# Kernel optimization log

Measured on AMD Instinct MI355X. Metric: run time of the kernel, lower is better.

Reference implementation:

```python
import jax, jax.numpy as jnp
import numpy as np

B, CIN, T, H, W = 4, 3, 32, 64, 64
COUT = 64


def setup_inputs() -> dict:
    key = jax.random.key(0)
    ks = jax.random.split(key, 6)
    X = jax.random.normal(ks[0], (B, CIN, T, H, W), jnp.float32)
    # Conv3d weight (O, I, D, kH, kW) for kernel (2,3,3)
    Wconv = jax.random.normal(ks[1], (4 * COUT, CIN, 2, 3, 3), jnp.float32) * 0.1
    bconv = jax.random.normal(ks[2], (4 * COUT,), jnp.float32) * 0.1
    # QRNNCell peephole params, shape (out_channels, *frame_size)
    W_ci = jax.random.normal(ks[3], (COUT, H, W), jnp.float32) * 0.1
    W_cf = jax.random.normal(ks[4], (COUT, H, W), jnp.float32) * 0.1
    W_co = jax.random.normal(ks[5], (COUT, H, W), jnp.float32) * 0.1
    return {"X": X, "Wconv": Wconv, "bconv": bconv,
            "W_ci": W_ci, "W_cf": W_cf, "W_co": W_co}


def reference(X, Wconv, bconv, W_ci, W_cf, W_co):
    # ConstantPad3d((1,1,1,1,1,0)): W +-1, H +-1, time front +1
    Xp = jnp.pad(X, ((0, 0), (0, 0), (1, 0), (1, 1), (1, 1)))
    # Conv3d, kernel (2,3,3), VALID -> output (B, 4*COUT, T, H, W)
    E = jax.lax.conv_general_dilated(
        Xp, Wconv, window_strides=(1, 1, 1), padding='VALID',
        dimension_numbers=('NCDHW', 'OIDHW', 'NCDHW'))
    E = E + bconv[None, :, None, None, None]
    i_c, f_c, g_c, o_c = jnp.split(E, 4, axis=1)  # each (B, COUT, T, H, W)
    # time-major stacked gates: (T, 4, B, COUT, H, W)
    gates = jnp.stack([jnp.moveaxis(x, 2, 0) for x in (i_c, f_c, g_c, o_c)], axis=1)

    def step(carry, g4):
        Hs, Cs = carry
        i, f, g, o = g4[0], g4[1], g4[2], g4[3]
        ig = jax.nn.sigmoid(i + W_ci * Cs)
        fg = jax.nn.sigmoid(f + W_cf * Cs)
        Cn = fg * Cs + ig * jnp.tanh(g)
        og = jax.nn.sigmoid(o + W_co * Cn)
        Hn = og * jnp.tanh(Cn)
        return (Hn, Cn), Hn

    z = jnp.zeros((X.shape[0], W_ci.shape[0], X.shape[3], X.shape[4]), X.dtype)
    _, outs = jax.lax.scan(step, (z, z), gates)  # outs: (T, B, COUT, H, W)
    return jnp.moveaxis(outs, 0, 2)  # (B, COUT, T, H, W)
```

## Files before the change

### kernel.cpp

```cpp
#include <hip/hip_runtime.h>

#define TT     32
#define HW     4096
#define LROW   68
#define LPLANE (6 * LROW)
#define SXSZ   (3 * LPLANE)
#define NSTG   (3 * 6 * 66)

__device__ __forceinline__ float fsigmoid(float x) {
    return __builtin_amdgcn_rcpf(1.0f + __builtin_amdgcn_exp2f(x * -1.4426950408889634f));
}
__device__ __forceinline__ float ftanh(float x) {
    return 2.0f * __builtin_amdgcn_rcpf(1.0f + __builtin_amdgcn_exp2f(x * -2.8853900817779268f)) - 1.0f;
}
__device__ __forceinline__ float sgprf(float v) {
    return __uint_as_float(__builtin_amdgcn_readfirstlane(__float_as_uint(v)));
}

__global__ __launch_bounds__(256, 4) void convqrnn(
    const float* __restrict__ X,
    const float* __restrict__ Wc,
    const float* __restrict__ bc,
    const float* __restrict__ Wci,
    const float* __restrict__ Wcf,
    const float* __restrict__ Wco,
    float* __restrict__ out)
{
    __shared__ float sx[2 * SXSZ];
    __shared__ float gb[2 * 1024];

    const int tid = threadIdx.x;
    const int h0  = blockIdx.x * 4;
    const int co  = blockIdx.y;
    const int b   = blockIdx.z;

    const int g  = tid >> 6;
    const int l  = tid & 63;
    const int r  = l >> 4;
    const int c0 = (l & 15) * 4;

    const int prow = tid >> 6;
    const int pcol = tid & 63;
    const int opix = (h0 + prow) * 64 + pcol;

    const float wci = Wci[co * HW + opix];
    const float wcf = Wcf[co * HW + opix];
    const float wco = Wco[co * HW + opix];

    float wgt[54];
    {
        const float* __restrict__ wrow = Wc + (size_t)(g * 64 + co) * 54;
        #pragma unroll
        for (int j = 0; j < 54; ++j) wgt[j] = sgprf(wrow[j]);
    }
    const float bg = sgprf(bc[g * 64 + co]);

    const float* __restrict__ Xb = X + (size_t)b * (3 * TT * HW);
    int soff[5];
    int goff[5];
    int svmask = 0;
    #pragma unroll
    for (int k = 0; k < 5; ++k) {
        int idx  = tid + k * 256;
        bool inr = (idx < NSTG);
        int idc  = inr ? idx : 0;
        int ci   = idc / 396;
        int rem  = idc - ci * 396;
        int y    = rem / 66;
        int x    = rem - y * 66;
        int gh   = h0 + y - 1;
        int gw   = x - 1;
        bool v   = inr && (gh >= 0) && (gh < 64) && (gw >= 0) && (gw < 64);
        int ghc  = gh < 0 ? 0 : (gh > 63 ? 63 : gh);
        int gwc  = gw < 0 ? 0 : (gw > 63 ? 63 : gw);
        soff[k]  = inr ? (ci * LPLANE + y * LROW + x) : (LROW - 1);
        goff[k]  = ci * (TT * HW) + ghc * 64 + gwc;
        svmask  |= (v ? 1 : 0) << k;
    }

    #pragma unroll
    for (int k = 0; k < 5; ++k) {
        float v = ((svmask >> k) & 1) ? Xb[goff[k]] : 0.0f;
        sx[soff[k]] = v;
        goff[k] += HW;
    }

    float* __restrict__ outb = out + (size_t)(b * 64 + co) * (TT * HW);
    int ooff = opix;

    float s0c0 = 0.f, s0c1 = 0.f, s0c2 = 0.f, s0c3 = 0.f;
    float C = 0.f;

    __syncthreads();

    for (int t = 0; t < TT; ++t) {
        const float* __restrict__ sxb = &sx[(t & 1) * SXSZ];
        float*       __restrict__ gbb = &gb[(t & 1) * 1024];

        float win[3][3][6];
        #pragma unroll
        for (int ci = 0; ci < 3; ++ci)
            #pragma unroll
            for (int kh = 0; kh < 3; ++kh) {
                const float* rowp = &sxb[ci * LPLANE + (r + kh) * LROW + c0];
                float4 lo = *(const float4*)rowp;
                float2 hi = *(const float2*)(rowp + 4);
                win[ci][kh][0] = lo.x; win[ci][kh][1] = lo.y;
                win[ci][kh][2] = lo.z; win[ci][kh][3] = lo.w;
                win[ci][kh][4] = hi.x; win[ci][kh][5] = hi.y;
            }

        float stv[5];
        if (t < TT - 1) {
            #pragma unroll
            for (int k = 0; k < 5; ++k) {
                stv[k] = ((svmask >> k) & 1) ? Xb[goff[k]] : 0.0f;
                goff[k] += HW;
            }
        }

        float s10 = bg, s11 = bg, s12 = bg, s13 = bg;
        float n0 = 0.f, n1 = 0.f, n2 = 0.f, n3 = 0.f;
        #pragma unroll
        for (int ci = 0; ci < 3; ++ci)
            #pragma unroll
            for (int kh = 0; kh < 3; ++kh)
                #pragma unroll
                for (int kw = 0; kw < 3; ++kw) {
                    const float wp = wgt[ci * 18 +     kh * 3 + kw];
                    const float wc = wgt[ci * 18 + 9 + kh * 3 + kw];
                    s10 += wc * win[ci][kh][kw + 0];
                    s11 += wc * win[ci][kh][kw + 1];
                    s12 += wc * win[ci][kh][kw + 2];
                    s13 += wc * win[ci][kh][kw + 3];
                    n0  += wp * win[ci][kh][kw + 0];
                    n1  += wp * win[ci][kh][kw + 1];
                    n2  += wp * win[ci][kh][kw + 2];
                    n3  += wp * win[ci][kh][kw + 3];
                }

        float4 gv = make_float4(s10 + s0c0, s11 + s0c1, s12 + s0c2, s13 + s0c3);
        s0c0 = n0; s0c1 = n1; s0c2 = n2; s0c3 = n3;
        *(float4*)&gbb[g * 256 + r * 64 + c0] = gv;

        if (t < TT - 1) {
            float* __restrict__ sxn = &sx[((t + 1) & 1) * SXSZ];
            #pragma unroll
            for (int k = 0; k < 5; ++k) sxn[soff[k]] = stv[k];
        }

        __syncthreads();

        const float iv = gbb[tid];
        const float fv = gbb[256 + tid];
        const float gg = gbb[512 + tid];
        const float ov = gbb[768 + tid];
        const float ig = fsigmoid(iv + wci * C);
        const float fg = fsigmoid(fv + wcf * C);
        const float Cn = fg * C + ig * ftanh(gg);
        const float og = fsigmoid(ov + wco * Cn);
        outb[ooff] = og * ftanh(Cn);
        ooff += HW;
        C = Cn;
    }
}

extern "C" void kernel_launch(void* const* d_in, const int* in_sizes, int n_in,
                              void* d_out, int out_size, void* d_ws, size_t ws_size,
                              hipStream_t stream) {
    const float* X   = (const float*)d_in[0];
    const float* Wc  = (const float*)d_in[1];
    const float* bc  = (const float*)d_in[2];
    const float* Wci = (const float*)d_in[3];
    const float* Wcf = (const float*)d_in[4];
    const float* Wco = (const float*)d_in[5];
    float* out = (float*)d_out;

    dim3 grid(16, 64, 4);
    convqrnn<<<grid, 256, 0, stream>>>(X, Wc, bc, Wci, Wcf, Wco, out);
}
```

Before: 462.7 us.

## Process two output channels per block to reuse staged input window

```diff
diff --git a/kernel.cpp b/kernel.cpp
--- a/kernel.cpp
+++ b/kernel.cpp
@@ -27,11 +27,11 @@
     float* __restrict__ out)
 {
     __shared__ float sx[2 * SXSZ];
-    __shared__ float gb[2 * 1024];
+    __shared__ float gb[2 * 2048];
 
     const int tid = threadIdx.x;
     const int h0  = blockIdx.x * 4;
-    const int co  = blockIdx.y;
+    const int co0 = blockIdx.y * 2;
     const int b   = blockIdx.z;
 
     const int g  = tid >> 6;
@@ -43,17 +43,24 @@
     const int pcol = tid & 63;
     const int opix = (h0 + prow) * 64 + pcol;
 
-    const float wci = Wci[co * HW + opix];
-    const float wcf = Wcf[co * HW + opix];
-    const float wco = Wco[co * HW + opix];
-
-    float wgt[54];
+    const float wciA = Wci[co0 * HW + opix];
+    const float wcfA = Wcf[co0 * HW + opix];
+    const float wcoA = Wco[co0 * HW + opix];
+    const float wciB = Wci[(co0 + 1) * HW + opix];
+    const float wcfB = Wcf[(co0 + 1) * HW + opix];
+    const float wcoB = Wco[(co0 + 1) * HW + opix];
+
+    float wgtA[54], wgtB[54];
     {
-        const float* __restrict__ wrow = Wc + (size_t)(g * 64 + co) * 54;
-        #pragma unroll
-        for (int j = 0; j < 54; ++j) wgt[j] = sgprf(wrow[j]);
-    }
-    const float bg = sgprf(bc[g * 64 + co]);
+        const float* __restrict__ wrA = Wc + (size_t)(g * 64 + co0) * 54;
+        const float* __restrict__ wrB = wrA + 54;
+        #pragma unroll
+        for (int j = 0; j < 54; ++j) wgtA[j] = sgprf(wrA[j]);
+        #pragma unroll
+        for (int j = 0; j < 54; ++j) wgtB[j] = sgprf(wrB[j]);
+    }
+    const float bgA = sgprf(bc[g * 64 + co0]);
+    const float bgB = sgprf(bc[g * 64 + co0 + 1]);
 
     const float* __restrict__ Xb = X + (size_t)b * (3 * TT * HW);
     int soff[5];
@@ -85,17 +92,19 @@
         goff[k] += HW;
     }
 
-    float* __restrict__ outb = out + (size_t)(b * 64 + co) * (TT * HW);
+    float* __restrict__ outA = out + (size_t)(b * 64 + co0) * (TT * HW);
+    float* __restrict__ outB = outA + (size_t)(TT * HW);
     int ooff = opix;
 
-    float s0c0 = 0.f, s0c1 = 0.f, s0c2 = 0.f, s0c3 = 0.f;
-    float C = 0.f;
+    float aA0 = 0.f, aA1 = 0.f, aA2 = 0.f, aA3 = 0.f;
+    float aB0 = 0.f, aB1 = 0.f, aB2 = 0.f, aB3 = 0.f;
+    float CA = 0.f, CB = 0.f;
 
     __syncthreads();
 
     for (int t = 0; t < TT; ++t) {
         const float* __restrict__ sxb = &sx[(t & 1) * SXSZ];
-        float*       __restrict__ gbb = &gb[(t & 1) * 1024];
+        float*       __restrict__ gbb = &gb[(t & 1) * 2048];
 
         float win[3][3][6];
         #pragma unroll
@@ -104,7 +113,7 @@
             for (int kh = 0; kh < 3; ++kh) {
                 const float* rowp = &sxb[ci * LPLANE + (r + kh) * LROW + c0];
                 float4 lo = *(const float4*)rowp;
-                float2 hi = *(const float2*)(rowp + 4);
+                float4 hi = *(const float4*)(rowp + 4);
                 win[ci][kh][0] = lo.x; win[ci][kh][1] = lo.y;
                 win[ci][kh][2] = lo.z; win[ci][kh][3] = lo.w;
                 win[ci][kh][4] = hi.x; win[ci][kh][5] = hi.y;
@@ -119,29 +128,40 @@
             }
         }
 
-        float s10 = bg, s11 = bg, s12 = bg, s13 = bg;
-        float n0 = 0.f, n1 = 0.f, n2 = 0.f, n3 = 0.f;
+        float sA0 = bgA, sA1 = bgA, sA2 = bgA, sA3 = bgA;
+        float sB0 = bgB, sB1 = bgB, sB2 = bgB, sB3 = bgB;
+        float nA0 = 0.f, nA1 = 0.f, nA2 = 0.f, nA3 = 0.f;
+        float nB0 = 0.f, nB1 = 0.f, nB2 = 0.f, nB3 = 0.f;
         #pragma unroll
         for (int ci = 0; ci < 3; ++ci)
             #pragma unroll
             for (int kh = 0; kh < 3; ++kh)
                 #pragma unroll
                 for (int kw = 0; kw < 3; ++kw) {
-                    const float wp = wgt[ci * 18 +     kh * 3 + kw];
-                    const float wc = wgt[ci * 18 + 9 + kh * 3 + kw];
-                    s10 += wc * win[ci][kh][kw + 0];
-                    s11 += wc * win[ci][kh][kw + 1];
-                    s12 += wc * win[ci][kh][kw + 2];
-                    s13 += wc * win[ci][kh][kw + 3];
-                    n0  += wp * win[ci][kh][kw + 0];
-                    n1  += wp * win[ci][kh][kw + 1];
-                    n2  += wp * win[ci][kh][kw + 2];
-                    n3  += wp * win[ci][kh][kw + 3];
+                    const float w0 = win[ci][kh][kw + 0];
+                    const float w1 = win[ci][kh][kw + 1];
+                    const float w2 = win[ci][kh][kw + 2];
+                    const float w3 = win[ci][kh][kw + 3];
+                    const float wpA = wgtA[ci * 18 +     kh * 3 + kw];
+                    const float wcA = wgtA[ci * 18 + 9 + kh * 3 + kw];
+                    const float wpB = wgtB[ci * 18 +     kh * 3 + kw];
+                    const float wcB = wgtB[ci * 18 + 9 + kh * 3 + kw];
+                    sA0 += wcA * w0;  sA1 += wcA * w1;
+                    sA2 += wcA * w2;  sA3 += wcA * w3;
+                    nA0 += wpA * w0;  nA1 += wpA * w1;
+                    nA2 += wpA * w2;  nA3 += wpA * w3;
+                    sB0 += wcB * w0;  sB1 += wcB * w1;
+                    sB2 += wcB * w2;  sB3 += wcB * w3;
+                    nB0 += wpB * w0;  nB1 += wpB * w1;
+                    nB2 += wpB * w2;  nB3 += wpB * w3;
                 }
 
-        float4 gv = make_float4(s10 + s0c0, s11 + s0c1, s12 + s0c2, s13 + s0c3);
-        s0c0 = n0; s0c1 = n1; s0c2 = n2; s0c3 = n3;
-        *(float4*)&gbb[g * 256 + r * 64 + c0] = gv;
+        float4 gvA = make_float4(sA0 + aA0, sA1 + aA1, sA2 + aA2, sA3 + aA3);
+        float4 gvB = make_float4(sB0 + aB0, sB1 + aB1, sB2 + aB2, sB3 + aB3);
+        aA0 = nA0; aA1 = nA1; aA2 = nA2; aA3 = nA3;
+        aB0 = nB0; aB1 = nB1; aB2 = nB2; aB3 = nB3;
+        *(float4*)&gbb[g * 256 + r * 64 + c0]        = gvA;
+        *(float4*)&gbb[1024 + g * 256 + r * 64 + c0] = gvB;
 
         if (t < TT - 1) {
             float* __restrict__ sxn = &sx[((t + 1) & 1) * SXSZ];
@@ -151,17 +171,31 @@
 
         __syncthreads();
 
-        const float iv = gbb[tid];
-        const float fv = gbb[256 + tid];
-        const float gg = gbb[512 + tid];
-        const float ov = gbb[768 + tid];
-        const float ig = fsigmoid(iv + wci * C);
-        const float fg = fsigmoid(fv + wcf * C);
-        const float Cn = fg * C + ig * ftanh(gg);
-        const float og = fsigmoid(ov + wco * Cn);
-        outb[ooff] = og * ftanh(Cn);
+        {
+            const float iv = gbb[tid];
+            const float fv = gbb[256 + tid];
+            const float gg = gbb[512 + tid];
+            const float ov = gbb[768 + tid];
+            const float ig = fsigmoid(iv + wciA * CA);
+            const float fg = fsigmoid(fv + wcfA * CA);
+            const float Cn = fg * CA + ig * ftanh(gg);
+            const float og = fsigmoid(ov + wcoA * Cn);
+            outA[ooff] = og * ftanh(Cn);
+            CA = Cn;
+        }
+        {
+            const float iv = gbb[1024 + tid];
+            const float fv = gbb[1024 + 256 + tid];
+            const float gg = gbb[1024 + 512 + tid];
+            const float ov = gbb[1024 + 768 + tid];
+            const float ig = fsigmoid(iv + wciB * CB);
+            const float fg = fsigmoid(fv + wcfB * CB);
+            const float Cn = fg * CB + ig * ftanh(gg);
+            const float og = fsigmoid(ov + wcoB * Cn);
+            outB[ooff] = og * ftanh(Cn);
+            CB = Cn;
+        }
         ooff += HW;
-        C = Cn;
     }
 }
 
@@ -176,6 +210,6 @@
     const float* Wco = (const float*)d_in[5];
     float* out = (float*)d_out;
 
-    dim3 grid(16, 64, 4);
+    dim3 grid(16, 32, 4);
     convqrnn<<<grid, 256, 0, stream>>>(X, Wc, bc, Wci, Wcf, Wco, out);
 }
```

New measurement: 438.7 us. 1.05x faster.

## Enlarge block tile to 8 rows and 2 output channels with 2-row register blocking

Applied to the files above, without the earlier changes.

```diff
diff --git a/kernel.cpp b/kernel.cpp
--- a/kernel.cpp
+++ b/kernel.cpp
@@ -3,9 +3,11 @@
 #define TT     32
 #define HW     4096
 #define LROW   68
-#define LPLANE (6 * LROW)
+#define NROWS  10
+#define LPLANE (NROWS * LROW)
 #define SXSZ   (3 * LPLANE)
-#define NSTG   (3 * 6 * 66)
+#define NSTG   (3 * NROWS * 66)
+#define GBSZ   4096
 
 __device__ __forceinline__ float fsigmoid(float x) {
     return __builtin_amdgcn_rcpf(1.0f + __builtin_amdgcn_exp2f(x * -1.4426950408889634f));
@@ -17,7 +19,7 @@
     return __uint_as_float(__builtin_amdgcn_readfirstlane(__float_as_uint(v)));
 }
 
-__global__ __launch_bounds__(256, 4) void convqrnn(
+__global__ __launch_bounds__(512, 2) void convqrnn(
     const float* __restrict__ X,
     const float* __restrict__ Wc,
     const float* __restrict__ bc,
@@ -27,25 +29,20 @@
     float* __restrict__ out)
 {
     __shared__ float sx[2 * SXSZ];
-    __shared__ float gb[2 * 1024];
+    __shared__ float gb[2 * GBSZ];
 
     const int tid = threadIdx.x;
-    const int h0  = blockIdx.x * 4;
-    const int co  = blockIdx.y;
+    const int h0  = blockIdx.x * 8;
+    const int co0 = blockIdx.y * 2;
     const int b   = blockIdx.z;
 
-    const int g  = tid >> 6;
+    const int w  = tid >> 6;
+    const int g  = w >> 1;
+    const int cA = w & 1;
+    const int co = co0 + cA;
     const int l  = tid & 63;
-    const int r  = l >> 4;
+    const int r2 = l >> 4;
     const int c0 = (l & 15) * 4;
-
-    const int prow = tid >> 6;
-    const int pcol = tid & 63;
-    const int opix = (h0 + prow) * 64 + pcol;
-
-    const float wci = Wci[co * HW + opix];
-    const float wcf = Wcf[co * HW + opix];
-    const float wco = Wco[co * HW + opix];
 
     float wgt[54];
     {
@@ -55,17 +52,26 @@
     }
     const float bg = sgprf(bc[g * 64 + co]);
 
+    const int cow = tid >> 8;
+    const int p2  = (tid & 255) * 2;
+    const int ppix = (co0 + cow) * HW + h0 * 64 + p2;
+    const float2 pwci = *(const float2*)&Wci[ppix];
+    const float2 pwcf = *(const float2*)&Wcf[ppix];
+    const float2 pwco = *(const float2*)&Wco[ppix];
+    float* __restrict__ outp =
+        out + (size_t)(b * 64 + co0 + cow) * (TT * HW) + h0 * 64 + p2;
+
     const float* __restrict__ Xb = X + (size_t)b * (3 * TT * HW);
-    int soff[5];
-    int goff[5];
+    int soff[4];
+    int goff[4];
     int svmask = 0;
     #pragma unroll
-    for (int k = 0; k < 5; ++k) {
-        int idx  = tid + k * 256;
+    for (int k = 0; k < 4; ++k) {
+        int idx  = tid + k * 512;
         bool inr = (idx < NSTG);
         int idc  = inr ? idx : 0;
-        int ci   = idc / 396;
-        int rem  = idc - ci * 396;
+        int ci   = idc / 660;
+        int rem  = idc - ci * 660;
         int y    = rem / 66;
         int x    = rem - y * 66;
         int gh   = h0 + y - 1;
@@ -73,95 +79,105 @@
         bool v   = inr && (gh >= 0) && (gh < 64) && (gw >= 0) && (gw < 64);
         int ghc  = gh < 0 ? 0 : (gh > 63 ? 63 : gh);
         int gwc  = gw < 0 ? 0 : (gw > 63 ? 63 : gw);
-        soff[k]  = inr ? (ci * LPLANE + y * LROW + x) : (LROW - 1);
+        soff[k]  = inr ? (ci * LPLANE + y * LROW + x) : 66;
         goff[k]  = ci * (TT * HW) + ghc * 64 + gwc;
         svmask  |= (v ? 1 : 0) << k;
     }
 
     #pragma unroll
-    for (int k = 0; k < 5; ++k) {
+    for (int k = 0; k < 4; ++k) {
         float v = ((svmask >> k) & 1) ? Xb[goff[k]] : 0.0f;
         sx[soff[k]] = v;
         goff[k] += HW;
     }
 
-    float* __restrict__ outb = out + (size_t)(b * 64 + co) * (TT * HW);
-    int ooff = opix;
-
-    float s0c0 = 0.f, s0c1 = 0.f, s0c2 = 0.f, s0c3 = 0.f;
-    float C = 0.f;
+    float na0 = 0.f, na1 = 0.f, na2 = 0.f, na3 = 0.f;
+    float nb0 = 0.f, nb1 = 0.f, nb2 = 0.f, nb3 = 0.f;
+    float Cc0 = 0.f, Cc1 = 0.f;
 
     __syncthreads();
 
     for (int t = 0; t < TT; ++t) {
         const float* __restrict__ sxb = &sx[(t & 1) * SXSZ];
-        float*       __restrict__ gbb = &gb[(t & 1) * 1024];
+        float*       __restrict__ gbb = &gb[(t & 1) * GBSZ];
 
-        float win[3][3][6];
-        #pragma unroll
-        for (int ci = 0; ci < 3; ++ci)
-            #pragma unroll
-            for (int kh = 0; kh < 3; ++kh) {
-                const float* rowp = &sxb[ci * LPLANE + (r + kh) * LROW + c0];
-                float4 lo = *(const float4*)rowp;
-                float2 hi = *(const float2*)(rowp + 4);
-                win[ci][kh][0] = lo.x; win[ci][kh][1] = lo.y;
-                win[ci][kh][2] = lo.z; win[ci][kh][3] = lo.w;
-                win[ci][kh][4] = hi.x; win[ci][kh][5] = hi.y;
-            }
+        float sa0 = bg + na0, sa1 = bg + na1, sa2 = bg + na2, sa3 = bg + na3;
+        float sb0 = bg + nb0, sb1 = bg + nb1, sb2 = bg + nb2, sb3 = bg + nb3;
+        na0 = na1 = na2 = na3 = 0.f;
+        nb0 = nb1 = nb2 = nb3 = 0.f;
 
-        float stv[5];
+        float stv[4];
         if (t < TT - 1) {
             #pragma unroll
-            for (int k = 0; k < 5; ++k) {
+            for (int k = 0; k < 4; ++k) {
                 stv[k] = ((svmask >> k) & 1) ? Xb[goff[k]] : 0.0f;
                 goff[k] += HW;
             }
         }
 
-        float s10 = bg, s11 = bg, s12 = bg, s13 = bg;
-        float n0 = 0.f, n1 = 0.f, n2 = 0.f, n3 = 0.f;
         #pragma unroll
-        for (int ci = 0; ci < 3; ++ci)
+        for (int ci = 0; ci < 3; ++ci) {
+            float wv[4][6];
+            #pragma unroll
+            for (int j = 0; j < 4; ++j) {
+                const float* rowp = &sxb[ci * LPLANE + (2 * r2 + j) * LROW + c0];
+                float4 lo = *(const float4*)rowp;
+                float2 hi = *(const float2*)(rowp + 4);
+                wv[j][0] = lo.x; wv[j][1] = lo.y; wv[j][2] = lo.z;
+                wv[j][3] = lo.w; wv[j][4] = hi.x; wv[j][5] = hi.y;
+            }
             #pragma unroll
             for (int kh = 0; kh < 3; ++kh)
                 #pragma unroll
                 for (int kw = 0; kw < 3; ++kw) {
                     const float wp = wgt[ci * 18 +     kh * 3 + kw];
                     const float wc = wgt[ci * 18 + 9 + kh * 3 + kw];
-                    s10 += wc * win[ci][kh][kw + 0];
-                    s11 += wc * win[ci][kh][kw + 1];
-                    s12 += wc * win[ci][kh][kw + 2];
-                    s13 += wc * win[ci][kh][kw + 3];
-                    n0  += wp * win[ci][kh][kw + 0];
-                    n1  += wp * win[ci][kh][kw + 1];
-                    n2  += wp * win[ci][kh][kw + 2];
-                    n3  += wp * win[ci][kh][kw + 3];
+                    sa0 += wc * wv[kh    ][kw + 0];  sa1 += wc * wv[kh    ][kw + 1];
+                    sa2 += wc * wv[kh    ][kw + 2];  sa3 += wc * wv[kh    ][kw + 3];
+                    sb0 += wc * wv[kh + 1][kw + 0];  sb1 += wc * wv[kh + 1][kw + 1];
+                    sb2 += wc * wv[kh + 1][kw + 2];  sb3 += wc * wv[kh + 1][kw + 3];
+                    na0 += wp * wv[kh    ][kw + 0];  na1 += wp * wv[kh    ][kw + 1];
+                    na2 += wp * wv[kh    ][kw + 2];  na3 += wp * wv[kh    ][kw + 3];
+                    nb0 += wp * wv[kh + 1][kw + 0];  nb1 += wp * wv[kh + 1][kw + 1];
+                    nb2 += wp * wv[kh + 1][kw + 2];  nb3 += wp * wv[kh + 1][kw + 3];
                 }
+        }
 
-        float4 gv = make_float4(s10 + s0c0, s11 + s0c1, s12 + s0c2, s13 + s0c3);
-        s0c0 = n0; s0c1 = n1; s0c2 = n2; s0c3 = n3;
-        *(float4*)&gbb[g * 256 + r * 64 + c0] = gv;
+        const int gbase = (cA * 4 + g) * 512 + (2 * r2) * 64 + c0;
+        *(float4*)&gbb[gbase]      = make_float4(sa0, sa1, sa2, sa3);
+        *(float4*)&gbb[gbase + 64] = make_float4(sb0, sb1, sb2, sb3);
 
         if (t < TT - 1) {
             float* __restrict__ sxn = &sx[((t + 1) & 1) * SXSZ];
             #pragma unroll
-            for (int k = 0; k < 5; ++k) sxn[soff[k]] = stv[k];
+            for (int k = 0; k < 4; ++k) sxn[soff[k]] = stv[k];
         }
 
         __syncthreads();
 
-        const float iv = gbb[tid];
-        const float fv = gbb[256 + tid];
-        const float gg = gbb[512 + tid];
-        const float ov = gbb[768 + tid];
-        const float ig = fsigmoid(iv + wci * C);
-        const float fg = fsigmoid(fv + wcf * C);
-        const float Cn = fg * C + ig * ftanh(gg);
-        const float og = fsigmoid(ov + wco * Cn);
-        outb[ooff] = og * ftanh(Cn);
-        ooff += HW;
-        C = Cn;
+        {
+            const int rb = cow * 4 * 512 + p2;
+            const float2 iv = *(const float2*)&gbb[rb];
+            const float2 fv = *(const float2*)&gbb[rb + 512];
+            const float2 gv = *(const float2*)&gbb[rb + 1024];
+            const float2 ov = *(const float2*)&gbb[rb + 1536];
+            float o0, o1;
+            {
+                const float ig = fsigmoid(iv.x + pwci.x * Cc0);
+                const float fg = fsigmoid(fv.x + pwcf.x * Cc0);
+                const float Cn = fg * Cc0 + ig * ftanh(gv.x);
+                const float og = fsigmoid(ov.x + pwco.x * Cn);
+                o0 = og * ftanh(Cn);  Cc0 = Cn;
+            }
+            {
+                const float ig = fsigmoid(iv.y + pwci.y * Cc1);
+                const float fg = fsigmoid(fv.y + pwcf.y * Cc1);
+                const float Cn = fg * Cc1 + ig * ftanh(gv.y);
+                const float og = fsigmoid(ov.y + pwco.y * Cn);
+                o1 = og * ftanh(Cn);  Cc1 = Cn;
+            }
+            *(float2*)&outp[t * HW] = make_float2(o0, o1);
+        }
     }
 }
 
@@ -176,6 +192,6 @@
     const float* Wco = (const float*)d_in[5];
     float* out = (float*)d_out;
 
-    dim3 grid(16, 64, 4);
-    convqrnn<<<grid, 256, 0, stream>>>(X, Wc, bc, Wci, Wcf, Wco, out);
+    dim3 grid(8, 32, 4);
+    convqrnn<<<grid, 512, 0, stream>>>(X, Wc, bc, Wci, Wcf, Wco, out);
 }
```

New measurement: 450.4 us. -2.7%, faster.
